# Optimization experiments

Hardware: AMD Instinct MI355X
Metric: run time of the kernel (lower is better)

## Reference

```python
import jax, jax.numpy as jnp
import numpy as np

N_NODES = 50000
N_EDGES = 800000
N_REL = 6
N_LAYERS = 8
D = 256
NUM_GRAPHS = 512


def setup_inputs() -> dict:
    key = jax.random.key(0)
    ks = jax.random.split(key, 24)
    s = lambda *sh: 1.0 / np.sqrt(sh[0])
    inp = {
        "x": jax.random.normal(ks[0], (N_NODES, 13), dtype=jnp.float32),
        "edge_index": jax.random.randint(ks[1], (2, N_EDGES), 0, N_NODES, dtype=jnp.int64),
        "edge_type": jax.random.randint(ks[2], (N_EDGES,), 0, N_REL, dtype=jnp.int64),
        "batch": jnp.sort(jax.random.randint(ks[3], (N_NODES,), 0, NUM_GRAPHS, dtype=jnp.int64)),
        "enc_W": jax.random.normal(ks[4], (13, D), dtype=jnp.float32) * s(13),
        "enc_b": jnp.zeros((D,), dtype=jnp.float32),
        "prelu_a": jnp.float32(0.25),
        "rel_W": jax.random.normal(ks[5], (N_LAYERS, N_REL, D, D), dtype=jnp.float32) * s(D),
        "root_W": jax.random.normal(ks[6], (N_LAYERS, D, D), dtype=jnp.float32) * s(D),
        "conv_b": jnp.zeros((N_LAYERS, D), dtype=jnp.float32),
        "gp_W1": jax.random.normal(ks[7], (D, D), dtype=jnp.float32) * s(D),
        "gp_b1": jnp.zeros((D,), dtype=jnp.float32),
        "gp_W2": jax.random.normal(ks[8], (D, D), dtype=jnp.float32) * s(D),
        "gp_b2": jnp.zeros((D,), dtype=jnp.float32),
        "fc_W1": jax.random.normal(ks[9], (D, 1024), dtype=jnp.float32) * s(D),
        "fc_b1": jnp.zeros((1024,), dtype=jnp.float32),
        "fc_W2": jax.random.normal(ks[10], (1024, 512), dtype=jnp.float32) * s(1024),
        "fc_b2": jnp.zeros((512,), dtype=jnp.float32),
        "out_W": jax.random.normal(ks[11], (512, 1), dtype=jnp.float32) * s(512),
        "out_b": jnp.zeros((1,), dtype=jnp.float32),
    }
    return inp


def reference(x, edge_index, edge_type, batch, enc_W, enc_b, prelu_a, rel_W, root_W,
              conv_b, gp_W1, gp_b1, gp_W2, gp_b2, fc_W1, fc_b1, fc_W2, fc_b2, out_W, out_b):
    src, dst = edge_index[0], edge_index[1]
    h = x @ enc_W + enc_b  # [N, D]
    for i in range(N_LAYERS):
        skip = h
        # per-relation transform for all nodes: [R, N, D]
        xW = jnp.einsum('nd,rde->rne', h, rel_W[i])
        msgs = xW[edge_type, src]  # [E, D] gather by (relation, source node)
        agg = jax.ops.segment_sum(msgs, dst, num_segments=N_NODES)
        h = agg + h @ root_W[i] + conv_b[i]
        h = h + skip
        h = jnp.where(h > 0, h, prelu_a * h)  # PReLU (shared scalar)
        norm = jnp.sqrt(jnp.sum(h * h, axis=1, keepdims=True))
        h = h / jnp.maximum(norm, 1e-12)  # F.normalize(p=2, dim=1)
    g = jax.nn.relu(h @ gp_W1 + gp_b1) @ gp_W2 + gp_b2
    pooled = jax.ops.segment_sum(g, batch, num_segments=NUM_GRAPHS)  # global_add_pool
    z = jax.nn.relu(pooled @ fc_W1 + fc_b1)  # dropout = identity at eval
    z = jax.nn.relu(z @ fc_W2 + fc_b2)
    return jax.nn.relu(z @ out_W + out_b)  # [NUM_GRAPHS, 1]
```

## Files before the change

### kernel.cpp

```cpp
#include <hip/hip_runtime.h>

#define N_NODES   50000
#define N_EDGES   800000
#define N_REL     6
#define N_LAYERS  8
#define DD        256
#define NUM_GRAPHS 512

#define NKEYS      (N_REL * N_NODES)
#define SCAN_T     256
#define SCAN_E     8
#define SCAN_CHUNK (SCAN_T * SCAN_E)
#define SCAN_NB    ((NKEYS + SCAN_CHUNK - 1) / SCAN_CHUNK)

typedef _Float16 h4 __attribute__((ext_vector_type(4)));
typedef _Float16 h8 __attribute__((ext_vector_type(8)));
typedef float    f4 __attribute__((ext_vector_type(4)));

__device__ __forceinline__ void atomAddF(float* p, float v) { unsafeAtomicAdd(p, v); }

__device__ __forceinline__ void load_lds16(const void* g, void* l) {
    __builtin_amdgcn_global_load_lds(
        (const __attribute__((address_space(1))) uint32_t*)g,
        (__attribute__((address_space(3))) uint32_t*)l, 16, 0, 0);
}

__global__ __launch_bounds__(256) void enc_kernel(const float* __restrict__ x,
                                                  const float* __restrict__ W,
                                                  const float* __restrict__ b,
                                                  _Float16* __restrict__ Hhi,
                                                  _Float16* __restrict__ Hlo) {
    int n = blockIdx.x;
    int d = threadIdx.x;
    float s = b[d];
#pragma unroll
    for (int k = 0; k < 13; ++k) s = fmaf(x[n * 13 + k], W[k * 256 + d], s);
    const _Float16 hi = (_Float16)s;
    Hhi[(size_t)n * DD + d] = hi;
    Hlo[(size_t)n * DD + d] = (_Float16)(s - (float)hi);
}

__global__ __launch_bounds__(256) void wsplit_rel_kernel(const float* __restrict__ relW,
                                                         const float* __restrict__ rootW,
                                                         _Float16* __restrict__ wthi,
                                                         _Float16* __restrict__ wtlo) {
    const size_t id = (size_t)blockIdx.x * 256 + threadIdx.x;
    if (id >= (size_t)N_LAYERS * 7 * 256 * 256) return;
    const int k = (int)(id & 255);
    const int n = (int)((id >> 8) & 255);
    const int g = (int)((id >> 16) % 7);
    const int L = (int)((id >> 16) / 7);
    float w = (g < 6)
        ? relW[(((size_t)L * 6 + g) * 256 + k) * 256 + n]
        : rootW[((size_t)L * 256 + k) * 256 + n];
    if (g == 6 && k == n) w += 1.0f;
    const _Float16 hi = (_Float16)w;
    const size_t o = ((size_t)L * 256 + n) * 1792 + (size_t)g * 256 + k;
    wthi[o] = hi;
    wtlo[o] = (_Float16)(w - (float)hi);
}

__global__ __launch_bounds__(256) void wsplit_tr_kernel(const float* __restrict__ W,
                                                        _Float16* __restrict__ whi,
                                                        _Float16* __restrict__ wlo,
                                                        int K, int N) {
    const size_t id = (size_t)blockIdx.x * 256 + threadIdx.x;
    if (id >= (size_t)K * N) return;
    const int k = (int)(id % K), n = (int)(id / K);
    const float w = W[(size_t)k * N + n];
    const _Float16 hi = (_Float16)w;
    whi[(size_t)n * K + k] = hi;
    wlo[(size_t)n * K + k] = (_Float16)(w - (float)hi);
}

__global__ __launch_bounds__(256) void fsplit_kernel(const float* __restrict__ S,
                                                     _Float16* __restrict__ hi,
                                                     _Float16* __restrict__ lo, int total) {
    const int id = blockIdx.x * 256 + threadIdx.x;
    if (id >= total) return;
    const float v = S[id];
    const _Float16 h = (_Float16)v;
    hi[id] = h;
    lo[id] = (_Float16)(v - (float)h);
}

template <int MODE>
__global__ __launch_bounds__(256, 2) void gemm_lds(
    const _Float16* __restrict__ Ahi, const _Float16* __restrict__ Alo,
    const _Float16* __restrict__ Hhi, const _Float16* __restrict__ Hlo,
    const _Float16* __restrict__ Bhi, const _Float16* __restrict__ Blo,
    int lda, int ldb, int ldc, int boff_agg, int boff_h, int K_agg, int K_tot,
    float* __restrict__ Cf, _Float16* __restrict__ Ohi, _Float16* __restrict__ Olo,
    const float* __restrict__ bias, const float* __restrict__ pa, int M) {
    __shared__ _Float16 smem[24576];
    const int lane = threadIdx.x & 63;
    const int wave = threadIdx.x >> 6;
    const int lm = lane & 15, lq = lane >> 4;
    const int wm = wave & 1, wn = wave >> 1;
    const int mb = blockIdx.x * 128;
    const int nb = blockIdx.y * 256;

    f4 acc[4][8];
#pragma unroll
    for (int i = 0; i < 4; ++i)
#pragma unroll
        for (int j = 0; j < 8; ++j) acc[i][j] = (f4){0.f, 0.f, 0.f, 0.f};

    for (int k0 = 0; k0 < K_tot; k0 += 32) {
        const _Float16 *pAh, *pAl;
        int acol, bcol;
        if (k0 < K_agg) {
            const size_t pb = (size_t)(k0 >> 8) * (size_t)N_NODES * DD;
            pAh = Ahi + pb; pAl = Alo + pb;
            acol = k0 & 255;
            bcol = boff_agg + k0;
        } else {
            pAh = Hhi; pAl = Hlo;
            acol = k0 - K_agg;
            bcol = boff_h + (k0 - K_agg);
        }

        __syncthreads();
#pragma unroll
        for (int q = 0; q < 12; ++q) {
            const int ub = (q * 4 + wave) * 64;
            const int u  = ub + lane;
            const _Float16* gp;
            size_t ga;
            if (q < 4) {
                const int v = u & 511, row = v >> 2, slot = v & 3;
                const int c = slot ^ ((row >> 1) & 3);
                int rg = mb + row; if (rg >= M) rg = M - 1;
                gp = (q < 2) ? pAh : pAl;
                ga = (size_t)rg * lda + acol + c * 8;
            } else {
                const int v = u & 1023, row = v >> 2, slot = v & 3;
                const int c = slot ^ ((row >> 1) & 3);
                gp = (q < 8) ? Bhi : Blo;
                ga = (size_t)(nb + row) * ldb + bcol + c * 8;
            }
            load_lds16(gp + ga, smem + (size_t)ub * 8);
        }
        __syncthreads();

        h8 ah[4], al[4], bh[8], bl[8];
#pragma unroll
        for (int i = 0; i < 4; ++i) {
            const int row  = wm * 64 + i * 16 + lm;
            const int slot = lq ^ ((row >> 1) & 3);
            const int o    = (row * 4 + slot) * 8;
            ah[i] = *(const h8*)(smem + o);
            al[i] = *(const h8*)(smem + 4096 + o);
        }
#pragma unroll
        for (int j = 0; j < 8; ++j) {
            const int n    = wn * 128 + j * 16 + lm;
            const int slot = lq ^ ((n >> 1) & 3);
            const int o    = (n * 4 + slot) * 8;
            bh[j] = *(const h8*)(smem + 8192 + o);
            bl[j] = *(const h8*)(smem + 16384 + o);
        }
#pragma unroll
        for (int i = 0; i < 4; ++i)
#pragma unroll
            for (int j = 0; j < 8; ++j) {
                acc[i][j] = __builtin_amdgcn_mfma_f32_16x16x32_f16(ah[i], bh[j], acc[i][j], 0, 0, 0);
                acc[i][j] = __builtin_amdgcn_mfma_f32_16x16x32_f16(ah[i], bl[j], acc[i][j], 0, 0, 0);
                acc[i][j] = __builtin_amdgcn_mfma_f32_16x16x32_f16(al[i], bh[j], acc[i][j], 0, 0, 0);
            }
    }

    if (MODE == 0) {
#pragma unroll
        for (int i = 0; i < 4; ++i)
#pragma unroll
            for (int r = 0; r < 4; ++r) {
                const int row = mb + wm * 64 + i * 16 + lq * 4 + r;
                if (row >= M) continue;
#pragma unroll
                for (int j = 0; j < 8; ++j) {
                    const int col = nb + wn * 128 + j * 16 + lm;
                    Cf[(size_t)row * ldc + col] = acc[i][j][r] + bias[col];
                }
            }
    } else if (MODE == 3) {
#pragma unroll
        for (int i = 0; i < 4; ++i)
#pragma unroll
            for (int r = 0; r < 4; ++r) {
                const int row = mb + wm * 64 + i * 16 + lq * 4 + r;
                if (row >= M) continue;
#pragma unroll
                for (int j = 0; j < 8; ++j) {
                    const int col = nb + wn * 128 + j * 16 + lm;
                    Cf[(size_t)row * ldc + col] += acc[i][j][r];
                }
            }
    } else if (MODE == 2) {
#pragma unroll
        for (int i = 0; i < 4; ++i)
#pragma unroll
            for (int r = 0; r < 4; ++r) {
                const int row = mb + wm * 64 + i * 16 + lq * 4 + r;
                if (row >= M) continue;
#pragma unroll
                for (int j = 0; j < 8; ++j) {
                    const int col = nb + wn * 128 + j * 16 + lm;
                    const float v = fmaxf(acc[i][j][r] + bias[col], 0.f);
                    const _Float16 hi = (_Float16)v;
                    const size_t idx = (size_t)row * ldc + col;
                    Ohi[idx] = hi;
                    Olo[idx] = (_Float16)(v - (float)hi);
                }
            }
    } else {
        float* shf = (float*)smem;
        const float a = pa[0];
        __syncthreads();
#pragma unroll
        for (int i = 0; i < 4; ++i)
#pragma unroll
            for (int r = 0; r < 4; ++r) {
                const int rl  = i * 16 + lq * 4 + r;
                const int row = mb + wm * 64 + rl;
                float rss = 0.f;
                if (row < M) {
#pragma unroll
                    for (int j = 0; j < 8; ++j) {
                        const int col = nb + wn * 128 + j * 16 + lm;
                        float v = acc[i][j][r] + Cf[(size_t)row * ldc + col];
                        v = v > 0.f ? v : a * v;
                        acc[i][j][r] = v;
                        rss = fmaf(v, v, rss);
                    }
                }
                rss += __shfl_xor(rss, 1, 64);
                rss += __shfl_xor(rss, 2, 64);
                rss += __shfl_xor(rss, 4, 64);
                rss += __shfl_xor(rss, 8, 64);
                if (lm == 0 && row < M) shf[wave * 64 + rl] = rss;
            }
        __syncthreads();
#pragma unroll
        for (int i = 0; i < 4; ++i)
#pragma unroll
            for (int r = 0; r < 4; ++r) {
                const int rl  = i * 16 + lq * 4 + r;
                const int row = mb + wm * 64 + rl;
                if (row >= M) continue;
                const float tot = shf[wm * 64 + rl] + shf[(2 + wm) * 64 + rl];
                const float inv = 1.0f / fmaxf(sqrtf(tot), 1e-12f);
#pragma unroll
                for (int j = 0; j < 8; ++j) {
                    const int col = nb + wn * 128 + j * 16 + lm;
                    const float v = acc[i][j][r] * inv;
                    const _Float16 hi = (_Float16)v;
                    const size_t idx = (size_t)row * ldc + col;
                    Ohi[idx] = hi;
                    Olo[idx] = (_Float16)(v - (float)hi);
                }
            }
    }
}

__global__ __launch_bounds__(256) void hist_kernel(const int* __restrict__ dst,
                                                   const int* __restrict__ etype,
                                                   int* __restrict__ cnt) {
    const int e = blockIdx.x * 256 + threadIdx.x;
    if (e >= N_EDGES) return;
    atomicAdd(&cnt[etype[e] * N_NODES + dst[e]], 1);
}

__global__ __launch_bounds__(SCAN_T) void scan1_kernel(const int* __restrict__ cnt,
                                                       int* __restrict__ off,
                                                       int* __restrict__ bsum) {
    __shared__ int sh[SCAN_T];
    const int b = blockIdx.x, t = threadIdx.x;
    const int base = b * SCAN_CHUNK + t * SCAN_E;
    int pre[SCAN_E];
    int s = 0;
#pragma unroll
    for (int i = 0; i < SCAN_E; ++i) {
        const int x = (base + i < NKEYS) ? cnt[base + i] : 0;
        pre[i] = s;
        s += x;
    }
    sh[t] = s;
    __syncthreads();
    for (int d = 1; d < SCAN_T; d <<= 1) {
        const int x = (t >= d) ? sh[t - d] : 0;
        __syncthreads();
        sh[t] += x;
        __syncthreads();
    }
    const int toff = (t == 0) ? 0 : sh[t - 1];
#pragma unroll
    for (int i = 0; i < SCAN_E; ++i)
        if (base + i < NKEYS) off[base + i] = toff + pre[i];
    if (t == SCAN_T - 1) bsum[b] = sh[SCAN_T - 1];
}

__global__ __launch_bounds__(SCAN_T) void scan2_kernel(int* __restrict__ bsum, int n) {
    __shared__ int sh[SCAN_T];
    const int t = threadIdx.x;
    const int base = t * SCAN_E;
    int pre[SCAN_E];
    int s = 0;
#pragma unroll
    for (int i = 0; i < SCAN_E; ++i) {
        const int x = (base + i < n) ? bsum[base + i] : 0;
        pre[i] = s;
        s += x;
    }
    sh[t] = s;
    __syncthreads();
    for (int d = 1; d < SCAN_T; d <<= 1) {
        const int x = (t >= d) ? sh[t - d] : 0;
        __syncthreads();
        sh[t] += x;
        __syncthreads();
    }
    const int toff = (t == 0) ? 0 : sh[t - 1];
#pragma unroll
    for (int i = 0; i < SCAN_E; ++i)
        if (base + i < n) bsum[base + i] = toff + pre[i];
}

__global__ __launch_bounds__(SCAN_T) void scan3_kernel(int* __restrict__ off,
                                                       const int* __restrict__ bsum) {
    const int b = blockIdx.x, t = threadIdx.x;
    const int add = bsum[b];
    const int base = b * SCAN_CHUNK + t * SCAN_E;
#pragma unroll
    for (int i = 0; i < SCAN_E; ++i)
        if (base + i < NKEYS) off[base + i] += add;
    if (b == 0 && t == 0) off[NKEYS] = N_EDGES;
}

__global__ __launch_bounds__(256) void csr_fill_kernel(const int* __restrict__ src,
                                                       const int* __restrict__ dst,
                                                       const int* __restrict__ etype,
                                                       int* __restrict__ cursor,
                                                       int* __restrict__ sorted_src) {
    const int e = blockIdx.x * 256 + threadIdx.x;
    if (e >= N_EDGES) return;
    const int key = etype[e] * N_NODES + dst[e];
    const int pos = atomicAdd(&cursor[key], 1);
    sorted_src[pos] = src[e];
}

__global__ __launch_bounds__(256) void agg2_kernel(const _Float16* __restrict__ Hhi,
                                                   const _Float16* __restrict__ Hlo,
                                                   const int* __restrict__ off,
                                                   const int* __restrict__ isrc,
                                                   _Float16* __restrict__ agghi,
                                                   _Float16* __restrict__ agglo, int rel0) {
    const int pair = blockIdx.x * 4 + (threadIdx.x >> 6);
    const int lane = threadIdx.x & 63;
    const int half = lane >> 5, li = lane & 31;
    if (pair >= 2 * N_NODES) return;
    const int rl   = (pair >= N_NODES) ? 1 : 0;
    const int node = pair - rl * N_NODES;
    const int r    = rel0 + rl;
    const int s0 = off[r * N_NODES + node];
    const int s1 = off[r * N_NODES + node + 1];
    float a[8] = {0.f, 0.f, 0.f, 0.f, 0.f, 0.f, 0.f, 0.f};
    for (int e0 = s0; e0 < s1; e0 += 2) {
        const int e = e0 + half;
        if (e < s1) {
            const int s = isrc[e];
            const h8 vh = *(const h8*)(Hhi + (size_t)s * DD + li * 8);
            const h8 vl = *(const h8*)(Hlo + (size_t)s * DD + li * 8);
#pragma unroll
            for (int k = 0; k < 8; ++k) a[k] += (float)vh[k] + (float)vl[k];
        }
    }
#pragma unroll
    for (int k = 0; k < 8; ++k) a[k] += __shfl_xor(a[k], 32, 64);
    if (half == 0) {
        h8 oh, ol;
#pragma unroll
        for (int k = 0; k < 8; ++k) {
            oh[k] = (_Float16)a[k];
            ol[k] = (_Float16)(a[k] - (float)oh[k]);
        }
        const size_t o = ((size_t)rl * N_NODES + node) * DD + li * 8;
        *(h8*)(agghi + o) = oh;
        *(h8*)(agglo + o) = ol;
    }
}

__global__ __launch_bounds__(64) void pool_kernel(const float* __restrict__ g,
                                                  const int* __restrict__ batch,
                                                  float* __restrict__ pooled) {
    const int c     = threadIdx.x;
    const int start = blockIdx.x * 128;
    const int end   = min(start + 128, N_NODES);
    int cur = batch[start];
    float4 acc = {0.f, 0.f, 0.f, 0.f};
    for (int n = start; n < end; ++n) {
        const int bn = batch[n];
        if (bn != cur) {
            float* p = pooled + (size_t)cur * DD + c * 4;
            atomAddF(p + 0, acc.x); atomAddF(p + 1, acc.y);
            atomAddF(p + 2, acc.z); atomAddF(p + 3, acc.w);
            acc = {0.f, 0.f, 0.f, 0.f};
            cur = bn;
        }
        const float4 v = reinterpret_cast<const float4*>(g + (size_t)n * DD)[c];
        acc.x += v.x; acc.y += v.y; acc.z += v.z; acc.w += v.w;
    }
    float* p = pooled + (size_t)cur * DD + c * 4;
    atomAddF(p + 0, acc.x); atomAddF(p + 1, acc.y);
    atomAddF(p + 2, acc.z); atomAddF(p + 3, acc.w);
}

__global__ __launch_bounds__(64) void out_kernel(const _Float16* __restrict__ z2hi,
                                                 const _Float16* __restrict__ z2lo,
                                                 const float* __restrict__ W,
                                                 const float* __restrict__ b,
                                                 float* __restrict__ out) {
    const int g = blockIdx.x;
    const int t = threadIdx.x;
    float s = 0.f;
#pragma unroll
    for (int j = 0; j < 8; ++j) {
        const int idx = t + 64 * j;
        const float z = (float)z2hi[(size_t)g * 512 + idx] + (float)z2lo[(size_t)g * 512 + idx];
        s = fmaf(z, W[idx], s);
    }
#pragma unroll
    for (int off = 32; off; off >>= 1) s += __shfl_xor(s, off, 64);
    if (t == 0) {
        const float v = s + b[0];
        out[g] = v > 0.f ? v : 0.f;
    }
}

extern "C" void kernel_launch(void* const* d_in, const int* in_sizes, int n_in,
                              void* d_out, int out_size, void* d_ws, size_t ws_size,
                              hipStream_t stream) {
    const float* x       = (const float*)d_in[0];
    const int*   eidx    = (const int*)d_in[1];
    const int*   etype   = (const int*)d_in[2];
    const int*   batch   = (const int*)d_in[3];
    const float* enc_W   = (const float*)d_in[4];
    const float* enc_b   = (const float*)d_in[5];
    const float* prelu_a = (const float*)d_in[6];
    const float* rel_W   = (const float*)d_in[7];
    const float* root_W  = (const float*)d_in[8];
    const float* conv_b  = (const float*)d_in[9];
    const float* gp_W1   = (const float*)d_in[10];
    const float* gp_b1   = (const float*)d_in[11];
    const float* gp_W2   = (const float*)d_in[12];
    const float* gp_b2   = (const float*)d_in[13];
    const float* fc_W1   = (const float*)d_in[14];
    const float* fc_b1   = (const float*)d_in[15];
    const float* fc_W2   = (const float*)d_in[16];
    const float* fc_b2   = (const float*)d_in[17];
    const float* out_W   = (const float*)d_in[18];
    const float* out_b   = (const float*)d_in[19];
    float* out = (float*)d_out;

    uint8_t* wp = (uint8_t*)d_ws;
    auto alloc = [&](size_t bytes) {
        void* r = (void*)wp;
        wp += (bytes + 255) & ~(size_t)255;
        return r;
    };
    float*    base   = (float*)alloc((size_t)N_NODES * DD * 4);
    _Float16* Hhi    = (_Float16*)alloc((size_t)N_NODES * DD * 2);
    _Float16* Hlo    = (_Float16*)alloc((size_t)N_NODES * DD * 2);
    _Float16* agghi  = (_Float16*)alloc((size_t)2 * N_NODES * DD * 2);
    _Float16* agglo  = (_Float16*)alloc((size_t)2 * N_NODES * DD * 2);
    _Float16* wthi   = (_Float16*)alloc((size_t)N_LAYERS * 256 * 1792 * 2);
    _Float16* wtlo   = (_Float16*)alloc((size_t)N_LAYERS * 256 * 1792 * 2);
    _Float16* wtg1hi = (_Float16*)alloc((size_t)256 * 256 * 2);
    _Float16* wtg1lo = (_Float16*)alloc((size_t)256 * 256 * 2);
    _Float16* wtg2hi = (_Float16*)alloc((size_t)256 * 256 * 2);
    _Float16* wtg2lo = (_Float16*)alloc((size_t)256 * 256 * 2);
    _Float16* wtf1hi = (_Float16*)alloc((size_t)1024 * 256 * 2);
    _Float16* wtf1lo = (_Float16*)alloc((size_t)1024 * 256 * 2);
    _Float16* wtf2hi = (_Float16*)alloc((size_t)512 * 1024 * 2);
    _Float16* wtf2lo = (_Float16*)alloc((size_t)512 * 1024 * 2);
    float*    pooled = (float*)alloc((size_t)NUM_GRAPHS * DD * 4);
    _Float16* phi    = (_Float16*)alloc((size_t)NUM_GRAPHS * DD * 2);
    _Float16* plo    = (_Float16*)alloc((size_t)NUM_GRAPHS * DD * 2);
    _Float16* z1hi   = (_Float16*)alloc((size_t)NUM_GRAPHS * 1024 * 2);
    _Float16* z1lo   = (_Float16*)alloc((size_t)NUM_GRAPHS * 1024 * 2);
    _Float16* z2hi   = (_Float16*)alloc((size_t)NUM_GRAPHS * 512 * 2);
    _Float16* z2lo   = (_Float16*)alloc((size_t)NUM_GRAPHS * 512 * 2);
    int*      ioff   = (int*)alloc((size_t)(NKEYS + 1) * 4);
    int*      icur   = (int*)alloc((size_t)NKEYS * 4);
    int*      ibsum  = (int*)alloc(256 * 4);
    int*      isrc   = (int*)alloc((size_t)N_EDGES * 4);

    const int* src = eidx;
    const int* dst = eidx + N_EDGES;

    const size_t wtot = (size_t)N_LAYERS * 7 * 256 * 256;
    wsplit_rel_kernel<<<(int)((wtot + 255) / 256), 256, 0, stream>>>(rel_W, root_W, wthi, wtlo);
    wsplit_tr_kernel<<<256, 256, 0, stream>>>(gp_W1, wtg1hi, wtg1lo, 256, 256);
    wsplit_tr_kernel<<<256, 256, 0, stream>>>(gp_W2, wtg2hi, wtg2lo, 256, 256);
    wsplit_tr_kernel<<<1024, 256, 0, stream>>>(fc_W1, wtf1hi, wtf1lo, 256, 1024);
    wsplit_tr_kernel<<<2048, 256, 0, stream>>>(fc_W2, wtf2hi, wtf2lo, 1024, 512);

    hipMemsetAsync(icur, 0, (size_t)NKEYS * sizeof(int), stream);
    const int eb = (N_EDGES + 255) / 256;
    hist_kernel<<<eb, 256, 0, stream>>>(dst, etype, icur);
    scan1_kernel<<<SCAN_NB, SCAN_T, 0, stream>>>(icur, ioff, ibsum);
    scan2_kernel<<<1, SCAN_T, 0, stream>>>(ibsum, SCAN_NB);
    scan3_kernel<<<SCAN_NB, SCAN_T, 0, stream>>>(ioff, ibsum);
    hipMemcpyAsync(icur, ioff, (size_t)NKEYS * sizeof(int), hipMemcpyDeviceToDevice, stream);
    csr_fill_kernel<<<eb, 256, 0, stream>>>(src, dst, etype, icur, isrc);

    enc_kernel<<<N_NODES, 256, 0, stream>>>(x, enc_W, enc_b, Hhi, Hlo);

    const dim3 gG((N_NODES + 127) / 128, 1);
    const int  aggb = (2 * N_NODES + 3) / 4;

    for (int L = 0; L < N_LAYERS; ++L) {
        const _Float16* Bh = wthi + (size_t)L * 256 * 1792;
        const _Float16* Bl = wtlo + (size_t)L * 256 * 1792;
        agg2_kernel<<<aggb, 256, 0, stream>>>(Hhi, Hlo, ioff, isrc, agghi, agglo, 0);
        gemm_lds<0><<<gG, 256, 0, stream>>>(agghi, agglo, Hhi, Hlo, Bh, Bl,
                                            256, 1792, 256, 0, 1536, 512, 768,
                                            base, nullptr, nullptr,
                                            conv_b + L * DD, nullptr, N_NODES);
        agg2_kernel<<<aggb, 256, 0, stream>>>(Hhi, Hlo, ioff, isrc, agghi, agglo, 2);
        gemm_lds<3><<<gG, 256, 0, stream>>>(agghi, agglo, Hhi, Hlo, Bh, Bl,
                                            256, 1792, 256, 512, 0, 512, 512,
                                            base, nullptr, nullptr,
                                            nullptr, nullptr, N_NODES);
        agg2_kernel<<<aggb, 256, 0, stream>>>(Hhi, Hlo, ioff, isrc, agghi, agglo, 4);
        gemm_lds<1><<<gG, 256, 0, stream>>>(agghi, agglo, Hhi, Hlo, Bh, Bl,
                                            256, 1792, 256, 1024, 0, 512, 512,
                                            base, Hhi, Hlo,
                                            nullptr, prelu_a, N_NODES);
    }

    gemm_lds<2><<<gG, 256, 0, stream>>>(nullptr, nullptr, Hhi, Hlo, wtg1hi, wtg1lo,
                                        256, 256, 256, 0, 0, 0, 256,
                                        nullptr, agghi, agglo, gp_b1, nullptr, N_NODES);
    gemm_lds<0><<<gG, 256, 0, stream>>>(agghi, agglo, nullptr, nullptr, wtg2hi, wtg2lo,
                                        256, 256, 256, 0, 0, 256, 256,
                                        base, nullptr, nullptr, gp_b2, nullptr, N_NODES);

    hipMemsetAsync(pooled, 0, (size_t)NUM_GRAPHS * DD * sizeof(float), stream);
    pool_kernel<<<(N_NODES + 127) / 128, 64, 0, stream>>>(base, batch, pooled);
    fsplit_kernel<<<(NUM_GRAPHS * DD + 255) / 256, 256, 0, stream>>>(
        pooled, phi, plo, NUM_GRAPHS * DD);

    gemm_lds<2><<<dim3(4, 4), 256, 0, stream>>>(nullptr, nullptr, phi, plo, wtf1hi, wtf1lo,
                                                256, 256, 1024, 0, 0, 0, 256,
                                                nullptr, z1hi, z1lo, fc_b1, nullptr,
                                                NUM_GRAPHS);
    gemm_lds<2><<<dim3(4, 2), 256, 0, stream>>>(nullptr, nullptr, z1hi, z1lo, wtf2hi, wtf2lo,
                                                1024, 1024, 512, 0, 0, 0, 1024,
                                                nullptr, z2hi, z2lo, fc_b2, nullptr,
                                                NUM_GRAPHS);
    out_kernel<<<NUM_GRAPHS, 64, 0, stream>>>(z2hi, z2lo, out_W, out_b, out);
}
```

Measured before the change: 3.194 ms.

## Shrink GEMM block tile to 64 rows for higher occupancy and precompute load addresses

The GEMM block tile drops from 128x256 to 64x256. Each wave now owns a 64x64 output slice, so the accumulator is 4x4 instead of 4x8, and launch bounds rise to 3 blocks per CU. The LDS global-load address math is hoisted out of the K loop, and the final gp_W2 GEMM now writes a half-precision hi/lo split that the pool kernel reads, instead of fp32. Smaller tiles give more blocks and waves to hide memory latency, at the cost of re-reading the B weights twice as often per output row.

```diff
diff --git a/kernel.cpp b/kernel.cpp
--- a/kernel.cpp
+++ b/kernel.cpp
@@ -85,26 +85,42 @@
 }
 
 template <int MODE>
-__global__ __launch_bounds__(256, 2) void gemm_lds(
+__global__ __launch_bounds__(256, 3) void gemm_lds(
     const _Float16* __restrict__ Ahi, const _Float16* __restrict__ Alo,
     const _Float16* __restrict__ Hhi, const _Float16* __restrict__ Hlo,
     const _Float16* __restrict__ Bhi, const _Float16* __restrict__ Blo,
     int lda, int ldb, int ldc, int boff_agg, int boff_h, int K_agg, int K_tot,
     float* __restrict__ Cf, _Float16* __restrict__ Ohi, _Float16* __restrict__ Olo,
     const float* __restrict__ bias, const float* __restrict__ pa, int M) {
-    __shared__ _Float16 smem[24576];
+    __shared__ _Float16 smem[20480];
     const int lane = threadIdx.x & 63;
     const int wave = threadIdx.x >> 6;
     const int lm = lane & 15, lq = lane >> 4;
-    const int wm = wave & 1, wn = wave >> 1;
-    const int mb = blockIdx.x * 128;
+    const int mb = blockIdx.x * 64;
     const int nb = blockIdx.y * 256;
 
-    f4 acc[4][8];
+    int arow_g, a_c8;
+    {
+        const int u = wave * 64 + lane;
+        const int row = u >> 2, slot = u & 3;
+        int rg = mb + row; if (rg >= M) rg = M - 1;
+        arow_g = rg;
+        a_c8   = (slot ^ ((row >> 1) & 3)) * 8;
+    }
+    int brow_g[4], b_c8[4];
+#pragma unroll
+    for (int q = 0; q < 4; ++q) {
+        const int u = q * 256 + wave * 64 + lane;
+        const int row = u >> 2, slot = u & 3;
+        brow_g[q] = nb + row;
+        b_c8[q]   = (slot ^ ((row >> 1) & 3)) * 8;
+    }
+
+    f4 acc[4][4];
 #pragma unroll
     for (int i = 0; i < 4; ++i)
 #pragma unroll
-        for (int j = 0; j < 8; ++j) acc[i][j] = (f4){0.f, 0.f, 0.f, 0.f};
+        for (int j = 0; j < 4; ++j) acc[i][j] = (f4){0.f, 0.f, 0.f, 0.f};
 
     for (int k0 = 0; k0 < K_tot; k0 += 32) {
         const _Float16 *pAh, *pAl;
@@ -121,49 +137,41 @@
         }
 
         __syncthreads();
-#pragma unroll
-        for (int q = 0; q < 12; ++q) {
-            const int ub = (q * 4 + wave) * 64;
-            const int u  = ub + lane;
-            const _Float16* gp;
-            size_t ga;
-            if (q < 4) {
-                const int v = u & 511, row = v >> 2, slot = v & 3;
-                const int c = slot ^ ((row >> 1) & 3);
-                int rg = mb + row; if (rg >= M) rg = M - 1;
-                gp = (q < 2) ? pAh : pAl;
-                ga = (size_t)rg * lda + acol + c * 8;
-            } else {
-                const int v = u & 1023, row = v >> 2, slot = v & 3;
-                const int c = slot ^ ((row >> 1) & 3);
-                gp = (q < 8) ? Bhi : Blo;
-                ga = (size_t)(nb + row) * ldb + bcol + c * 8;
-            }
-            load_lds16(gp + ga, smem + (size_t)ub * 8);
-        }
-        __syncthreads();
-
-        h8 ah[4], al[4], bh[8], bl[8];
+        {
+            const size_t ga = (size_t)arow_g * lda + acol + a_c8;
+            load_lds16(pAh + ga, smem + wave * 512);
+            load_lds16(pAl + ga, smem + 2048 + wave * 512);
+        }
+#pragma unroll
+        for (int q = 0; q < 4; ++q) {
+            const size_t gb = (size_t)brow_g[q] * ldb + bcol + b_c8[q];
+            const int eb = (q * 256 + wave * 64) * 8;
+            load_lds16(Bhi + gb, smem + 4096 + eb);
+            load_lds16(Blo + gb, smem + 12288 + eb);
+        }
+        __syncthreads();
+
+        h8 ah[4], al[4], bh[4], bl[4];
 #pragma unroll
         for (int i = 0; i < 4; ++i) {
-            const int row  = wm * 64 + i * 16 + lm;
+            const int row  = i * 16 + lm;
             const int slot = lq ^ ((row >> 1) & 3);
             const int o    = (row * 4 + slot) * 8;
             ah[i] = *(const h8*)(smem + o);
-            al[i] = *(const h8*)(smem + 4096 + o);
-        }
-#pragma unroll
-        for (int j = 0; j < 8; ++j) {
-            const int n    = wn * 128 + j * 16 + lm;
+            al[i] = *(const h8*)(smem + 2048 + o);
+        }
+#pragma unroll
+        for (int j = 0; j < 4; ++j) {
+            const int n    = wave * 64 + j * 16 + lm;
             const int slot = lq ^ ((n >> 1) & 3);
             const int o    = (n * 4 + slot) * 8;
-            bh[j] = *(const h8*)(smem + 8192 + o);
-            bl[j] = *(const h8*)(smem + 16384 + o);
+            bh[j] = *(const h8*)(smem + 4096 + o);
+            bl[j] = *(const h8*)(smem + 12288 + o);
         }
 #pragma unroll
         for (int i = 0; i < 4; ++i)
 #pragma unroll
-            for (int j = 0; j < 8; ++j) {
+            for (int j = 0; j < 4; ++j) {
                 acc[i][j] = __builtin_amdgcn_mfma_f32_16x16x32_f16(ah[i], bh[j], acc[i][j], 0, 0, 0);
                 acc[i][j] = __builtin_amdgcn_mfma_f32_16x16x32_f16(ah[i], bl[j], acc[i][j], 0, 0, 0);
                 acc[i][j] = __builtin_amdgcn_mfma_f32_16x16x32_f16(al[i], bh[j], acc[i][j], 0, 0, 0);
@@ -175,11 +183,11 @@
         for (int i = 0; i < 4; ++i)
 #pragma unroll
             for (int r = 0; r < 4; ++r) {
-                const int row = mb + wm * 64 + i * 16 + lq * 4 + r;
+                const int row = mb + i * 16 + lq * 4 + r;
                 if (row >= M) continue;
 #pragma unroll
-                for (int j = 0; j < 8; ++j) {
-                    const int col = nb + wn * 128 + j * 16 + lm;
+                for (int j = 0; j < 4; ++j) {
+                    const int col = nb + wave * 64 + j * 16 + lm;
                     Cf[(size_t)row * ldc + col] = acc[i][j][r] + bias[col];
                 }
             }
@@ -188,25 +196,26 @@
         for (int i = 0; i < 4; ++i)
 #pragma unroll
             for (int r = 0; r < 4; ++r) {
-                const int row = mb + wm * 64 + i * 16 + lq * 4 + r;
+                const int row = mb + i * 16 + lq * 4 + r;
                 if (row >= M) continue;
 #pragma unroll
-                for (int j = 0; j < 8; ++j) {
-                    const int col = nb + wn * 128 + j * 16 + lm;
+                for (int j = 0; j < 4; ++j) {
+                    const int col = nb + wave * 64 + j * 16 + lm;
                     Cf[(size_t)row * ldc + col] += acc[i][j][r];
                 }
             }
-    } else if (MODE == 2) {
+    } else if (MODE == 2 || MODE == 4) {
 #pragma unroll
         for (int i = 0; i < 4; ++i)
 #pragma unroll
             for (int r = 0; r < 4; ++r) {
-                const int row = mb + wm * 64 + i * 16 + lq * 4 + r;
+                const int row = mb + i * 16 + lq * 4 + r;
                 if (row >= M) continue;
 #pragma unroll
-                for (int j = 0; j < 8; ++j) {
-                    const int col = nb + wn * 128 + j * 16 + lm;
-                    const float v = fmaxf(acc[i][j][r] + bias[col], 0.f);
+                for (int j = 0; j < 4; ++j) {
+                    const int col = nb + wave * 64 + j * 16 + lm;
+                    float v = acc[i][j][r] + bias[col];
+                    if (MODE == 2) v = fmaxf(v, 0.f);
                     const _Float16 hi = (_Float16)v;
                     const size_t idx = (size_t)row * ldc + col;
                     Ohi[idx] = hi;
@@ -222,12 +231,12 @@
 #pragma unroll
             for (int r = 0; r < 4; ++r) {
                 const int rl  = i * 16 + lq * 4 + r;
-                const int row = mb + wm * 64 + rl;
+                const int row = mb + rl;
                 float rss = 0.f;
                 if (row < M) {
 #pragma unroll
-                    for (int j = 0; j < 8; ++j) {
-                        const int col = nb + wn * 128 + j * 16 + lm;
+                    for (int j = 0; j < 4; ++j) {
+                        const int col = nb + wave * 64 + j * 16 + lm;
                         float v = acc[i][j][r] + Cf[(size_t)row * ldc + col];
                         v = v > 0.f ? v : a * v;
                         acc[i][j][r] = v;
@@ -246,13 +255,13 @@
 #pragma unroll
             for (int r = 0; r < 4; ++r) {
                 const int rl  = i * 16 + lq * 4 + r;
-                const int row = mb + wm * 64 + rl;
+                const int row = mb + rl;
                 if (row >= M) continue;
-                const float tot = shf[wm * 64 + rl] + shf[(2 + wm) * 64 + rl];
+                const float tot = shf[rl] + shf[64 + rl] + shf[128 + rl] + shf[192 + rl];
                 const float inv = 1.0f / fmaxf(sqrtf(tot), 1e-12f);
 #pragma unroll
-                for (int j = 0; j < 8; ++j) {
-                    const int col = nb + wn * 128 + j * 16 + lm;
+                for (int j = 0; j < 4; ++j) {
+                    const int col = nb + wave * 64 + j * 16 + lm;
                     const float v = acc[i][j][r] * inv;
                     const _Float16 hi = (_Float16)v;
                     const size_t idx = (size_t)row * ldc + col;
@@ -349,19 +358,20 @@
     sorted_src[pos] = src[e];
 }
 
-__global__ __launch_bounds__(256) void agg2_kernel(const _Float16* __restrict__ Hhi,
-                                                   const _Float16* __restrict__ Hlo,
-                                                   const int* __restrict__ off,
-                                                   const int* __restrict__ isrc,
-                                                   _Float16* __restrict__ agghi,
-                                                   _Float16* __restrict__ agglo, int rel0) {
-    const int pair = blockIdx.x * 4 + (threadIdx.x >> 6);
+__global__ __launch_bounds__(256) void agg_kernel(const _Float16* __restrict__ Hhi,
+                                                  const _Float16* __restrict__ Hlo,
+                                                  const int* __restrict__ off,
+                                                  const int* __restrict__ isrc,
+                                                  _Float16* __restrict__ agghi,
+                                                  _Float16* __restrict__ agglo,
+                                                  int rel0, int nrel) {
+    const int p    = blockIdx.x * 4 + (threadIdx.x >> 6);
     const int lane = threadIdx.x & 63;
     const int half = lane >> 5, li = lane & 31;
-    if (pair >= 2 * N_NODES) return;
-    const int rl   = (pair >= N_NODES) ? 1 : 0;
-    const int node = pair - rl * N_NODES;
-    const int r    = rel0 + rl;
+    if (p >= nrel * N_NODES) return;
+    const int pl   = p / N_NODES;
+    const int node = p - pl * N_NODES;
+    const int r    = rel0 + pl;
     const int s0 = off[r * N_NODES + node];
     const int s1 = off[r * N_NODES + node + 1];
     float a[8] = {0.f, 0.f, 0.f, 0.f, 0.f, 0.f, 0.f, 0.f};
@@ -384,13 +394,14 @@
             oh[k] = (_Float16)a[k];
             ol[k] = (_Float16)(a[k] - (float)oh[k]);
         }
-        const size_t o = ((size_t)rl * N_NODES + node) * DD + li * 8;
+        const size_t o = ((size_t)pl * N_NODES + node) * DD + li * 8;
         *(h8*)(agghi + o) = oh;
         *(h8*)(agglo + o) = ol;
     }
 }
 
-__global__ __launch_bounds__(64) void pool_kernel(const float* __restrict__ g,
+__global__ __launch_bounds__(64) void pool_kernel(const _Float16* __restrict__ ghi,
+                                                  const _Float16* __restrict__ glo,
                                                   const int* __restrict__ batch,
                                                   float* __restrict__ pooled) {
     const int c     = threadIdx.x;
@@ -407,8 +418,12 @@
             acc = {0.f, 0.f, 0.f, 0.f};
             cur = bn;
         }
-        const float4 v = reinterpret_cast<const float4*>(g + (size_t)n * DD)[c];
-        acc.x += v.x; acc.y += v.y; acc.z += v.z; acc.w += v.w;
+        const h4 vh = *(const h4*)(ghi + (size_t)n * DD + c * 4);
+        const h4 vl = *(const h4*)(glo + (size_t)n * DD + c * 4);
+        acc.x += (float)vh[0] + (float)vl[0];
+        acc.y += (float)vh[1] + (float)vl[1];
+        acc.z += (float)vh[2] + (float)vl[2];
+        acc.w += (float)vh[3] + (float)vl[3];
     }
     float* p = pooled + (size_t)cur * DD + c * 4;
     atomAddF(p + 0, acc.x); atomAddF(p + 1, acc.y);
@@ -516,24 +531,24 @@
 
     enc_kernel<<<N_NODES, 256, 0, stream>>>(x, enc_W, enc_b, Hhi, Hlo);
 
-    const dim3 gG((N_NODES + 127) / 128, 1);
+    const dim3 gG((N_NODES + 63) / 64, 1);
     const int  aggb = (2 * N_NODES + 3) / 4;
 
     for (int L = 0; L < N_LAYERS; ++L) {
         const _Float16* Bh = wthi + (size_t)L * 256 * 1792;
         const _Float16* Bl = wtlo + (size_t)L * 256 * 1792;
-        agg2_kernel<<<aggb, 256, 0, stream>>>(Hhi, Hlo, ioff, isrc, agghi, agglo, 0);
+        agg_kernel<<<aggb, 256, 0, stream>>>(Hhi, Hlo, ioff, isrc, agghi, agglo, 0, 2);
         gemm_lds<0><<<gG, 256, 0, stream>>>(agghi, agglo, Hhi, Hlo, Bh, Bl,
                                             256, 1792, 256, 0, 1536, 512, 768,
                                             base, nullptr, nullptr,
                                             conv_b + L * DD, nullptr, N_NODES);
-        agg2_kernel<<<aggb, 256, 0, stream>>>(Hhi, Hlo, ioff, isrc, agghi, agglo, 2);
-        gemm_lds<3><<<gG, 256, 0, stream>>>(agghi, agglo, Hhi, Hlo, Bh, Bl,
+        agg_kernel<<<aggb, 256, 0, stream>>>(Hhi, Hlo, ioff, isrc, agghi, agglo, 2, 2);
+        gemm_lds<3><<<gG, 256, 0, stream>>>(agghi, agglo, nullptr, nullptr, Bh, Bl,
                                             256, 1792, 256, 512, 0, 512, 512,
                                             base, nullptr, nullptr,
                                             nullptr, nullptr, N_NODES);
-        agg2_kernel<<<aggb, 256, 0, stream>>>(Hhi, Hlo, ioff, isrc, agghi, agglo, 4);
-        gemm_lds<1><<<gG, 256, 0, stream>>>(agghi, agglo, Hhi, Hlo, Bh, Bl,
+        agg_kernel<<<aggb, 256, 0, stream>>>(Hhi, Hlo, ioff, isrc, agghi, agglo, 4, 2);
+        gemm_lds<1><<<gG, 256, 0, stream>>>(agghi, agglo, nullptr, nullptr, Bh, Bl,
                                             256, 1792, 256, 1024, 0, 512, 512,
                                             base, Hhi, Hlo,
                                             nullptr, prelu_a, N_NODES);
@@ -542,20 +557,22 @@
     gemm_lds<2><<<gG, 256, 0, stream>>>(nullptr, nullptr, Hhi, Hlo, wtg1hi, wtg1lo,
                                         256, 256, 256, 0, 0, 0, 256,
                                         nullptr, agghi, agglo, gp_b1, nullptr, N_NODES);
-    gemm_lds<0><<<gG, 256, 0, stream>>>(agghi, agglo, nullptr, nullptr, wtg2hi, wtg2lo,
-                                        256, 256, 256, 0, 0, 256, 256,
-                                        base, nullptr, nullptr, gp_b2, nullptr, N_NODES);
+    gemm_lds<4><<<gG, 256, 0, stream>>>(nullptr, nullptr, agghi, agglo, wtg2hi, wtg2lo,
+                                        256, 256, 256, 0, 0, 0, 256,
+                                        nullptr, agghi + (size_t)N_NODES * DD,
+                                        agglo + (size_t)N_NODES * DD, gp_b2, nullptr, N_NODES);
 
     hipMemsetAsync(pooled, 0, (size_t)NUM_GRAPHS * DD * sizeof(float), stream);
-    pool_kernel<<<(N_NODES + 127) / 128, 64, 0, stream>>>(base, batch, pooled);
+    pool_kernel<<<(N_NODES + 127) / 128, 64, 0, stream>>>(
+        agghi + (size_t)N_NODES * DD, agglo + (size_t)N_NODES * DD, batch, pooled);
     fsplit_kernel<<<(NUM_GRAPHS * DD + 255) / 256, 256, 0, stream>>>(
         pooled, phi, plo, NUM_GRAPHS * DD);
 
-    gemm_lds<2><<<dim3(4, 4), 256, 0, stream>>>(nullptr, nullptr, phi, plo, wtf1hi, wtf1lo,
+    gemm_lds<2><<<dim3(8, 4), 256, 0, stream>>>(nullptr, nullptr, phi, plo, wtf1hi, wtf1lo,
                                                 256, 256, 1024, 0, 0, 0, 256,
                                                 nullptr, z1hi, z1lo, fc_b1, nullptr,
                                                 NUM_GRAPHS);
-    gemm_lds<2><<<dim3(4, 2), 256, 0, stream>>>(nullptr, nullptr, z1hi, z1lo, wtf2hi, wtf2lo,
+    gemm_lds<2><<<dim3(8, 2), 256, 0, stream>>>(nullptr, nullptr, z1hi, z1lo, wtf2hi, wtf2lo,
                                                 1024, 1024, 512, 0, 0, 0, 1024,
                                                 nullptr, z2hi, z2lo, fc_b2, nullptr,
                                                 NUM_GRAPHS);
```

Result: slower. 3.611 ms (+13.0%).
